# Kernel tuning notes

Measured on AMD Instinct MI355X. Metric: run time of the kernel, lower is better.

Reference implementation:

```python
import jax, jax.numpy as jnp
import numpy as np

N_NODES = 100000
N_EDGES = 1600000
IN_DIM = 128
HID_DIM = 128
OUT_DIM = 64
BN_EPS = 1e-5


def setup_inputs() -> dict:
    key = jax.random.key(0)
    ks = jax.random.split(key, 8)
    x = jax.random.normal(ks[0], (N_NODES, IN_DIM), dtype=jnp.float32)
    edge_index = jax.random.randint(ks[1], (2, N_EDGES), 0, N_NODES, dtype=jnp.int64)
    s1 = 1.0 / np.sqrt(IN_DIM)
    s2 = 1.0 / np.sqrt(HID_DIM)
    return {
        "x": x,
        "edge_index": edge_index,
        "W1l": jax.random.normal(ks[2], (HID_DIM, IN_DIM), dtype=jnp.float32) * s1,
        "b1l": jnp.zeros((HID_DIM,), dtype=jnp.float32),
        "W1r": jax.random.normal(ks[3], (HID_DIM, IN_DIM), dtype=jnp.float32) * s1,
        "bn_gamma": jnp.ones((HID_DIM,), dtype=jnp.float32),
        "bn_beta": jnp.zeros((HID_DIM,), dtype=jnp.float32),
        "bn_mean": jnp.zeros((HID_DIM,), dtype=jnp.float32),
        "bn_var": jnp.ones((HID_DIM,), dtype=jnp.float32),
        "W2l": jax.random.normal(ks[4], (OUT_DIM, HID_DIM), dtype=jnp.float32) * s2,
        "b2l": jnp.zeros((OUT_DIM,), dtype=jnp.float32),
        "W2r": jax.random.normal(ks[5], (OUT_DIM, HID_DIM), dtype=jnp.float32) * s2,
    }


def _sage_conv(x, src, dst, Wl, bl, Wr, num_nodes):
    # message = x[src], mean-aggregated at dst; out = lin_l(agg) + lin_r(x)
    msgs = x[src]  # [E, D] gather (memory bound)
    agg = jax.ops.segment_sum(msgs, dst, num_segments=num_nodes)
    deg = jax.ops.segment_sum(jnp.ones((src.shape[0],), dtype=x.dtype), dst,
                              num_segments=num_nodes)
    agg = agg / jnp.maximum(deg, 1.0)[:, None]
    return agg @ Wl.T + bl + x @ Wr.T


def reference(x, edge_index, W1l, b1l, W1r, bn_gamma, bn_beta, bn_mean, bn_var,
              W2l, b2l, W2r):
    src, dst = edge_index[0], edge_index[1]
    n = x.shape[0]
    h = _sage_conv(x, src, dst, W1l, b1l, W1r, n)
    # BatchNorm1d (inference: running stats), then ReLU; dropout is identity in eval
    h = (h - bn_mean) * (bn_gamma * jax.lax.rsqrt(bn_var + BN_EPS)) + bn_beta
    h = jax.nn.relu(h)
    return _sage_conv(h, src, dst, W2l, b2l, W2r, n)
```

## Files before the change

kernel.cpp:

```cpp
#include <hip/hip_runtime.h>
#include <hip/hip_fp16.h>

#define N_NODES 100000
#define N_EDGES 1600000
#define TILE 2048
#define NBUK 64
#define BSH 11
#define NBUK_USED ((N_NODES + (1 << BSH) - 1) >> BSH)
#define CAP 36864
#define SMASK 0x1FFFF

typedef _Float16 f16x8 __attribute__((ext_vector_type(8)));
typedef float    f32x4 __attribute__((ext_vector_type(4)));

__global__ __launch_bounds__(256) void k_pre(
    const float* __restrict__ x, __half* __restrict__ x_h,
    const float* __restrict__ W1l, const float* __restrict__ W1r,
    const float* __restrict__ W2l, const float* __restrict__ W2r,
    __half* __restrict__ W1lf, __half* __restrict__ W1rf,
    __half* __restrict__ W2f, int* __restrict__ bcur)
{
    int i = blockIdx.x * 256 + threadIdx.x;
    if (i < N_NODES * 32) {
        float4 v = ((const float4*)x)[i];
        __half2 a = __floats2half2_rn(v.x, v.y);
        __half2 b = __floats2half2_rn(v.z, v.w);
        uint2 u = make_uint2(*(unsigned*)&a, *(unsigned*)&b);
        ((uint2*)x_h)[i] = u;
    }
    if (i < 49152) {
        int tt = i & 16383;
        int j    = tt & 7;
        int lane = (tt >> 3) & 63;
        int ks   = (tt >> 9) & 3;
        int ct   = tt >> 11;
        int m = lane & 15, q = lane >> 4;
        int row = ct * 16 + m;
        int col = ks * 32 + q * 8 + j;
        if (i < 16384) {
            W1lf[tt] = __float2half(W1l[row * 128 + col]);
        } else if (i < 32768) {
            W1rf[tt] = __float2half(W1r[row * 128 + col]);
        } else {
            float v = (ct < 4) ? W2l[row * 128 + col]
                               : W2r[(row - 64) * 128 + col];
            W2f[tt] = __float2half(v);
        }
    }
    if (i < NBUK) bcur[i] = i * CAP;
}

__global__ __launch_bounds__(256) void k_binA(
    const int* __restrict__ ei, int* __restrict__ bcur,
    int2* __restrict__ ebuf)
{
    __shared__ int2 scratch[TILE];
    __shared__ int hist[NBUK];
    __shared__ int tstart[NBUK];
    __shared__ int gbase[NBUK];
    int t = threadIdx.x;
    int e0 = blockIdx.x * TILE;
    int tile_n = min(TILE, N_EDGES - e0);
    if (t < NBUK) hist[t] = 0;
    __syncthreads();
    int srcs[8], dsts[8], rank[8], bks[8];
    #pragma unroll
    for (int i = 0; i < 8; ++i) {
        int e = e0 + i * 256 + t;
        bks[i] = -1;
        if (e < N_EDGES) {
            srcs[i] = ei[e];
            dsts[i] = ei[N_EDGES + e];
            bks[i]  = (dsts[i] >> BSH) & (NBUK - 1);
            rank[i] = atomicAdd(&hist[bks[i]], 1);
        }
    }
    __syncthreads();
    if (t == 0) {
        int s = 0;
        #pragma unroll
        for (int b = 0; b < NBUK; ++b) { tstart[b] = s; s += hist[b]; }
    }
    __syncthreads();
    if (t < NBUK && hist[t] > 0)
        gbase[t] = atomicAdd(&bcur[t], hist[t]);
    __syncthreads();
    #pragma unroll
    for (int i = 0; i < 8; ++i)
        if (bks[i] >= 0) {
            int sl = tstart[bks[i]] + rank[i];
            scratch[min(sl, TILE - 1)] = make_int2(srcs[i], dsts[i]);
        }
    __syncthreads();
    for (int p = t; p < tile_n; p += 256) {
        int2 sd = scratch[p];
        int b = (sd.y >> BSH) & (NBUK - 1);
        int o = gbase[b] + (p - tstart[b]);
        ebuf[min(max(o, 0), NBUK * CAP - 1)] = sd;
    }
}

__global__ __launch_bounds__(1024) void k_fillC2(
    const int2* __restrict__ ebuf, const int* __restrict__ bcur,
    int* __restrict__ row_ptr, int* __restrict__ csr_src)
{
    __shared__ int hist[1 << BSH];
    __shared__ int psum[1024];
    __shared__ int cur[1 << BSH];
    __shared__ int bb_l[NBUK_USED + 1];
    int t = threadIdx.x;
    int b = blockIdx.x;
    int base = b << BSH;
    hist[t] = 0;
    hist[t + 1024] = 0;
    if (t < 64) {
        int c = (t < NBUK_USED) ? (bcur[t] - t * CAP) : 0;
        c = min(max(c, 0), CAP);
        int s = c;
        #pragma unroll
        for (int off = 1; off < 64; off <<= 1) {
            int v = __shfl_up(s, off);
            if (t >= off) s += v;
        }
        if (t < NBUK_USED) bb_l[t] = s - c;
        if (t == NBUK_USED - 1) bb_l[NBUK_USED] = s;
    }
    __syncthreads();
    int bb  = bb_l[b];
    int cnt = min(bb_l[b + 1] - bb, CAP);
    const int2* eb = ebuf + (size_t)b * CAP;
    for (int p = t; p < cnt; p += 1024)
        atomicAdd(&hist[(eb[p].y - base) & ((1 << BSH) - 1)], 1);
    __syncthreads();
    int h0 = hist[2 * t], h1 = hist[2 * t + 1];
    psum[t] = h0 + h1;
    __syncthreads();
    #pragma unroll
    for (int off = 1; off < 1024; off <<= 1) {
        int v = (t >= off) ? psum[t - off] : 0;
        __syncthreads();
        psum[t] += v;
        __syncthreads();
    }
    int e0 = bb + psum[t] - (h0 + h1);
    int e1 = e0 + h0;
    int n0g = base + 2 * t, n1g = n0g + 1;
    if (n0g <= N_NODES) row_ptr[n0g] = e0;
    if (n1g <= N_NODES) row_ptr[n1g] = e1;
    cur[2 * t]     = e0;
    cur[2 * t + 1] = e1;
    __syncthreads();
    for (int p = t; p < cnt; p += 1024) {
        int2 sd = eb[p];
        int pos = atomicAdd(&cur[(sd.y - base) & ((1 << BSH) - 1)], 1);
        csr_src[min(max(pos, 0), N_EDGES - 1)] = sd.x;
    }
}

__device__ __forceinline__ void acc_row8(
    const __half* __restrict__ x_h, int s, int col, float4& acc)
{
    uint2 u = ((const uint2*)(x_h + (size_t)(s & SMASK) * 128))[col];
    __half2 a = *(__half2*)&u.x;
    __half2 b = *(__half2*)&u.y;
    float2 fa = __half22float2(a);
    float2 fb = __half22float2(b);
    acc.x += fa.x; acc.y += fa.y; acc.z += fb.x; acc.w += fb.y;
}

__global__ __launch_bounds__(256) void k_l12(
    const int* __restrict__ row_ptr, const int* __restrict__ csr_src,
    const __half* __restrict__ x_h,
    const __half* __restrict__ W1lf, const float* __restrict__ b1l,
    const __half* __restrict__ W1rf,
    const float* __restrict__ gamma, const float* __restrict__ beta,
    const float* __restrict__ mean, const float* __restrict__ var,
    const __half* __restrict__ W2f, const float* __restrict__ b2l,
    __half* __restrict__ p2, float* __restrict__ out)
{
    __shared__ char sm[34816];
    __half (*Aagg)[64][8] = (__half(*)[64][8])sm;
    __half (*Ax)[64][8]   = (__half(*)[64][8])(sm + 16384);
    __half (*Ah)[64][8]   = (__half(*)[64][8])sm;
    float  (*Cs)[132]     = (float(*)[132])sm;
    __shared__ float invdeg[64];
    int tid  = threadIdx.x;
    int lane = tid & 63;
    int w    = tid >> 6;
    int n0   = blockIdx.x * 64;

    {
        int n  = tid & 63;
        int kg = tid >> 6;
        int ng = n0 + n;
        const uint4* px = (const uint4*)(x_h + (size_t)ng * 128 + kg * 32);
        #pragma unroll
        for (int i = 0; i < 4; ++i) {
            uint4 vx = make_uint4(0, 0, 0, 0);
            if (ng < N_NODES) vx = px[i];
            *(uint4*)&Ax[kg * 4 + i][n][0] = vx;
        }
    }

    {
        int half = lane >> 5;
        int col  = lane & 31;
        for (int i = 0; i < 16; ++i) {
            int nn = n0 + w * 16 + i;
            int e0 = 0, e1 = 0;
            if (nn < N_NODES) {
                e1 = min(row_ptr[nn + 1], N_EDGES);
                e0 = min(max(row_ptr[nn], 0), e1);
            }
            float4 acc = make_float4(0.f, 0.f, 0.f, 0.f);
            for (int eb = e0; eb < e1; eb += 64) {
                int cnt = min(e1 - eb, 64);
                int sv = csr_src[min(eb + lane, N_EDGES - 1)];
                int j = 0;
                for (; j + 8 <= cnt; j += 8) {
                    #pragma unroll
                    for (int u = 0; u < 4; ++u) {
                        int sa = __builtin_amdgcn_readlane(sv, j + 2 * u);
                        int sb = __builtin_amdgcn_readlane(sv, j + 2 * u + 1);
                        int s  = half ? sb : sa;
                        acc_row8(x_h, s, col, acc);
                    }
                }
                for (; j + 2 <= cnt; j += 2) {
                    int sa = __builtin_amdgcn_readlane(sv, j);
                    int sb = __builtin_amdgcn_readlane(sv, j + 1);
                    int s  = half ? sb : sa;
                    acc_row8(x_h, s, col, acc);
                }
                if (j < cnt) {
                    int sa = __builtin_amdgcn_readlane(sv, j);
                    if (half == 0) acc_row8(x_h, sa, col, acc);
                }
            }
            acc.x += __shfl_xor(acc.x, 32);
            acc.y += __shfl_xor(acc.y, 32);
            acc.z += __shfl_xor(acc.z, 32);
            acc.w += __shfl_xor(acc.w, 32);
            if (lane == 0)
                invdeg[w * 16 + i] = 1.0f / fmaxf((float)(e1 - e0), 1.0f);
            if (half == 0) {
                __half2 h0 = __floats2half2_rn(acc.x, acc.y);
                __half2 h1 = __floats2half2_rn(acc.z, acc.w);
                uint2 u = make_uint2(*(unsigned*)&h0, *(unsigned*)&h1);
                *(uint2*)&Aagg[col >> 1][w * 16 + i][(col & 1) * 4] = u;
            }
        }
    }
    __syncthreads();

    int m = lane & 15;
    int q = lane >> 4;
    int row = w * 16 + m;
    const __half* bl0 = W1lf + (lane << 3);
    const __half* br0 = W1rf + (lane << 3);
    f32x4 accL[8], accR[8];
    #pragma unroll
    for (int c = 0; c < 8; ++c) {
        accL[c] = (f32x4){0.f, 0.f, 0.f, 0.f};
        accR[c] = (f32x4){0.f, 0.f, 0.f, 0.f};
    }
    #pragma unroll
    for (int ks = 0; ks < 4; ++ks) {
        f16x8 aL = *(const f16x8*)&Aagg[ks * 4 + q][row][0];
        f16x8 aR = *(const f16x8*)&Ax[ks * 4 + q][row][0];
        #pragma unroll
        for (int ct = 0; ct < 8; ++ct) {
            f16x8 bL = *(const f16x8*)(bl0 + ((ct * 4 + ks) << 9));
            f16x8 bR = *(const f16x8*)(br0 + ((ct * 4 + ks) << 9));
            accL[ct] = __builtin_amdgcn_mfma_f32_16x16x32_f16(aL, bL, accL[ct], 0, 0, 0);
            accR[ct] = __builtin_amdgcn_mfma_f32_16x16x32_f16(aR, bR, accR[ct], 0, 0, 0);
        }
    }
    float invd[4];
    #pragma unroll
    for (int r = 0; r < 4; ++r)
        invd[r] = invdeg[w * 16 + q * 4 + r];
    __syncthreads();

    #pragma unroll
    for (int ct = 0; ct < 8; ++ct) {
        int col = ct * 16 + m;
        float s = gamma[col] * rsqrtf(var[col] + 1e-5f);
        float t = beta[col] + (b1l[col] - mean[col]) * s;
        #pragma unroll
        for (int r = 0; r < 4; ++r) {
            float v = accL[ct][r] * invd[r] + accR[ct][r];
            v = fmaxf(v * s + t, 0.f);
            Ah[col >> 3][w * 16 + q * 4 + r][col & 7] = __float2half(v);
        }
    }
    __syncthreads();

    const __half* b0 = W2f + (lane << 3);
    f32x4 acc2[8];
    #pragma unroll
    for (int c = 0; c < 8; ++c) acc2[c] = (f32x4){0.f, 0.f, 0.f, 0.f};
    #pragma unroll
    for (int ks = 0; ks < 4; ++ks) {
        f16x8 a = *(const f16x8*)&Ah[ks * 4 + q][row][0];
        #pragma unroll
        for (int ct = 0; ct < 8; ++ct) {
            f16x8 b = *(const f16x8*)(b0 + ((ct * 4 + ks) << 9));
            acc2[ct] = __builtin_amdgcn_mfma_f32_16x16x32_f16(a, b, acc2[ct], 0, 0, 0);
        }
    }
    __syncthreads();
    #pragma unroll
    for (int ct = 0; ct < 8; ++ct) {
        int col = ct * 16 + m;
        #pragma unroll
        for (int r = 0; r < 4; ++r)
            Cs[w * 16 + q * 4 + r][col] = acc2[ct][r];
    }
    __syncthreads();
    {
        int rr = tid & 63;
        int pg = tid >> 6;
        int ng = n0 + rr;
        if (ng < N_NODES) {
            union { __half hh[16]; uint4 u[2]; } tmp;
            #pragma unroll
            for (int c = 0; c < 16; ++c)
                tmp.hh[c] = __float2half(Cs[rr][pg * 16 + c]);
            uint4* dp = (uint4*)(p2 + (size_t)ng * 64 + pg * 16);
            dp[0] = tmp.u[0];
            dp[1] = tmp.u[1];
            #pragma unroll
            for (int i = 0; i < 4; ++i) {
                float4 v  = *(const float4*)&Cs[rr][64 + pg * 16 + i * 4];
                float4 bb = *(const float4*)(b2l + pg * 16 + i * 4);
                v.x += bb.x; v.y += bb.y; v.z += bb.z; v.w += bb.w;
                *(float4*)(out + (size_t)ng * 64 + pg * 16 + i * 4) = v;
            }
        }
    }
}

__device__ __forceinline__ void acc_row_p2(
    const __half* __restrict__ p2, int s, int lane, float4& acc)
{
    uint2 u = ((const uint2*)(p2 + (size_t)(s & SMASK) * 64))[lane];
    __half2 a = *(__half2*)&u.x;
    __half2 b = *(__half2*)&u.y;
    float2 fa = __half22float2(a);
    float2 fb = __half22float2(b);
    acc.x += fa.x; acc.y += fa.y; acc.z += fb.x; acc.w += fb.y;
}

__global__ __launch_bounds__(256) void k_agg2(
    const int* __restrict__ row_ptr, const int* __restrict__ csr_src,
    const __half* __restrict__ p2, float* __restrict__ out)
{
    int tid  = threadIdx.x;
    int n    = blockIdx.x * 16 + (tid >> 4);
    int lane = tid & 15;
    int e1 = min(row_ptr[n + 1], N_EDGES);
    int e0 = min(max(row_ptr[n], 0), e1);
    float4 acc = make_float4(0.f, 0.f, 0.f, 0.f);
    int e = e0;
    for (; e + 4 <= e1; e += 4) {
        int s0 = csr_src[e], s1 = csr_src[e + 1];
        int s2 = csr_src[e + 2], s3 = csr_src[e + 3];
        acc_row_p2(p2, s0, lane, acc);
        acc_row_p2(p2, s1, lane, acc);
        acc_row_p2(p2, s2, lane, acc);
        acc_row_p2(p2, s3, lane, acc);
    }
    for (; e < e1; ++e) acc_row_p2(p2, csr_src[e], lane, acc);
    float inv = 1.0f / fmaxf((float)(e1 - e0), 1.0f);
    float4* o = (float4*)out + n * 16 + lane;
    float4 cur = *o;
    cur.x += acc.x * inv; cur.y += acc.y * inv;
    cur.z += acc.z * inv; cur.w += acc.w * inv;
    *o = cur;
}

extern "C" void kernel_launch(void* const* d_in, const int* in_sizes, int n_in,
                              void* d_out, int out_size, void* d_ws, size_t ws_size,
                              hipStream_t stream)
{
    const float* x     = (const float*)d_in[0];
    const int*   ei    = (const int*)d_in[1];
    const float* W1l   = (const float*)d_in[2];
    const float* b1l   = (const float*)d_in[3];
    const float* W1r   = (const float*)d_in[4];
    const float* gamma = (const float*)d_in[5];
    const float* beta  = (const float*)d_in[6];
    const float* mean  = (const float*)d_in[7];
    const float* var   = (const float*)d_in[8];
    const float* W2l   = (const float*)d_in[9];
    const float* b2l   = (const float*)d_in[10];
    const float* W2r   = (const float*)d_in[11];
    float* out = (float*)d_out;

    char* ws = (char*)d_ws;
    __half* p2      = (__half*)(ws);
    __half* x_h     = (__half*)(ws + 51200000);
    int*    csr_src = (int*)(ws + 76800000);
    int*    row_ptr = (int*)(ws + 83200000);
    __half* W1lf    = (__half*)(ws + 83600016);
    __half* W1rf    = (__half*)(ws + 83632784);
    __half* W2f     = (__half*)(ws + 83665552);
    int2*   ebuf    = (int2*)(ws + 83698320);
    int*    bcur    = (int*)(ws + 102572688);

    k_pre<<<12500, 256, 0, stream>>>(x, x_h, W1l, W1r, W2l, W2r,
                                     W1lf, W1rf, W2f, bcur);
    k_binA<<<(N_EDGES + TILE - 1) / TILE, 256, 0, stream>>>(ei, bcur, ebuf);
    k_fillC2<<<NBUK_USED, 1024, 0, stream>>>(ebuf, bcur, row_ptr, csr_src);
    k_l12<<<(N_NODES + 63) / 64, 256, 0, stream>>>(row_ptr, csr_src, x_h,
                                                   W1lf, b1l, W1rf,
                                                   gamma, beta, mean, var,
                                                   W2f, b2l, p2, out);
    k_agg2<<<N_NODES / 16, 256, 0, stream>>>(row_ptr, csr_src, p2, out);
}
```

Before: 378.7 us.

## Split layer-1 aggregation out of fused GEMM kernel into separate gather kernel

Moves the layer-1 neighbor gather out of the fused aggregate+GEMM kernel into a standalone kernel with one wave per node and many small blocks, writing fp16 aggregates to a workspace buffer. The GEMM kernel then loads the aggregates coalesced and recomputes inverse degree from row_ptr. The aim is better latency hiding and load balance for the gather, since it no longer runs serially 16 nodes per wave inside a shared-memory-heavy block. The cost is an extra 25.6MB write and read plus one more kernel launch.

```diff
diff --git a/kernel.cpp b/kernel.cpp
--- a/kernel.cpp
+++ b/kernel.cpp
@@ -168,8 +168,56 @@
     acc.x += fa.x; acc.y += fa.y; acc.z += fb.x; acc.w += fb.y;
 }
 
-__global__ __launch_bounds__(256) void k_l12(
+__global__ __launch_bounds__(256) void k_agg1(
     const int* __restrict__ row_ptr, const int* __restrict__ csr_src,
+    const __half* __restrict__ x_h, __half* __restrict__ agg_h)
+{
+    int tid  = threadIdx.x;
+    int lane = tid & 63;
+    int half = lane >> 5;
+    int col  = lane & 31;
+    int n    = blockIdx.x * 4 + (tid >> 6);
+    int e1 = min(row_ptr[n + 1], N_EDGES);
+    int e0 = min(max(row_ptr[n], 0), e1);
+    float4 acc = make_float4(0.f, 0.f, 0.f, 0.f);
+    for (int eb = e0; eb < e1; eb += 64) {
+        int cnt = min(e1 - eb, 64);
+        int sv = csr_src[min(eb + lane, N_EDGES - 1)];
+        int j = 0;
+        for (; j + 8 <= cnt; j += 8) {
+            #pragma unroll
+            for (int u = 0; u < 4; ++u) {
+                int sa = __builtin_amdgcn_readlane(sv, j + 2 * u);
+                int sb = __builtin_amdgcn_readlane(sv, j + 2 * u + 1);
+                int s  = half ? sb : sa;
+                acc_row8(x_h, s, col, acc);
+            }
+        }
+        for (; j + 2 <= cnt; j += 2) {
+            int sa = __builtin_amdgcn_readlane(sv, j);
+            int sb = __builtin_amdgcn_readlane(sv, j + 1);
+            int s  = half ? sb : sa;
+            acc_row8(x_h, s, col, acc);
+        }
+        if (j < cnt) {
+            int sa = __builtin_amdgcn_readlane(sv, j);
+            if (half == 0) acc_row8(x_h, sa, col, acc);
+        }
+    }
+    acc.x += __shfl_xor(acc.x, 32);
+    acc.y += __shfl_xor(acc.y, 32);
+    acc.z += __shfl_xor(acc.z, 32);
+    acc.w += __shfl_xor(acc.w, 32);
+    if (half == 0) {
+        __half2 h0 = __floats2half2_rn(acc.x, acc.y);
+        __half2 h1 = __floats2half2_rn(acc.z, acc.w);
+        uint2 u = make_uint2(*(unsigned*)&h0, *(unsigned*)&h1);
+        ((uint2*)agg_h)[n * 32 + col] = u;
+    }
+}
+
+__global__ __launch_bounds__(256) void k_g12(
+    const __half* __restrict__ agg_h, const int* __restrict__ row_ptr,
     const __half* __restrict__ x_h,
     const __half* __restrict__ W1lf, const float* __restrict__ b1l,
     const __half* __restrict__ W1rf,
@@ -183,76 +231,27 @@
     __half (*Ax)[64][8]   = (__half(*)[64][8])(sm + 16384);
     __half (*Ah)[64][8]   = (__half(*)[64][8])sm;
     float  (*Cs)[132]     = (float(*)[132])sm;
-    __shared__ float invdeg[64];
-    int tid  = threadIdx.x;
-    int lane = tid & 63;
-    int w    = tid >> 6;
-    int n0   = blockIdx.x * 64;
+    int tid = threadIdx.x;
+    int n0  = blockIdx.x * 64;
 
     {
         int n  = tid & 63;
         int kg = tid >> 6;
         int ng = n0 + n;
-        const uint4* px = (const uint4*)(x_h + (size_t)ng * 128 + kg * 32);
+        const uint4* pa = (const uint4*)(agg_h + (size_t)ng * 128 + kg * 32);
+        const uint4* px = (const uint4*)(x_h   + (size_t)ng * 128 + kg * 32);
         #pragma unroll
         for (int i = 0; i < 4; ++i) {
-            uint4 vx = make_uint4(0, 0, 0, 0);
-            if (ng < N_NODES) vx = px[i];
-            *(uint4*)&Ax[kg * 4 + i][n][0] = vx;
-        }
-    }
-
-    {
-        int half = lane >> 5;
-        int col  = lane & 31;
-        for (int i = 0; i < 16; ++i) {
-            int nn = n0 + w * 16 + i;
-            int e0 = 0, e1 = 0;
-            if (nn < N_NODES) {
-                e1 = min(row_ptr[nn + 1], N_EDGES);
-                e0 = min(max(row_ptr[nn], 0), e1);
-            }
-            float4 acc = make_float4(0.f, 0.f, 0.f, 0.f);
-            for (int eb = e0; eb < e1; eb += 64) {
-                int cnt = min(e1 - eb, 64);
-                int sv = csr_src[min(eb + lane, N_EDGES - 1)];
-                int j = 0;
-                for (; j + 8 <= cnt; j += 8) {
-                    #pragma unroll
-                    for (int u = 0; u < 4; ++u) {
-                        int sa = __builtin_amdgcn_readlane(sv, j + 2 * u);
-                        int sb = __builtin_amdgcn_readlane(sv, j + 2 * u + 1);
-                        int s  = half ? sb : sa;
-                        acc_row8(x_h, s, col, acc);
-                    }
-                }
-                for (; j + 2 <= cnt; j += 2) {
-                    int sa = __builtin_amdgcn_readlane(sv, j);
-                    int sb = __builtin_amdgcn_readlane(sv, j + 1);
-                    int s  = half ? sb : sa;
-                    acc_row8(x_h, s, col, acc);
-                }
-                if (j < cnt) {
-                    int sa = __builtin_amdgcn_readlane(sv, j);
-                    if (half == 0) acc_row8(x_h, sa, col, acc);
-                }
-            }
-            acc.x += __shfl_xor(acc.x, 32);
-            acc.y += __shfl_xor(acc.y, 32);
-            acc.z += __shfl_xor(acc.z, 32);
-            acc.w += __shfl_xor(acc.w, 32);
-            if (lane == 0)
-                invdeg[w * 16 + i] = 1.0f / fmaxf((float)(e1 - e0), 1.0f);
-            if (half == 0) {
-                __half2 h0 = __floats2half2_rn(acc.x, acc.y);
-                __half2 h1 = __floats2half2_rn(acc.z, acc.w);
-                uint2 u = make_uint2(*(unsigned*)&h0, *(unsigned*)&h1);
-                *(uint2*)&Aagg[col >> 1][w * 16 + i][(col & 1) * 4] = u;
-            }
-        }
-    }
-    __syncthreads();
-
+            uint4 va = make_uint4(0, 0, 0, 0), vx = va;
+            if (ng < N_NODES) { va = pa[i]; vx = px[i]; }
+            *(uint4*)&Aagg[kg * 4 + i][n][0] = va;
+            *(uint4*)&Ax[kg * 4 + i][n][0]   = vx;
+        }
+    }
+    __syncthreads();
+
+    int lane = tid & 63;
+    int w = tid >> 6;
     int m = lane & 15;
     int q = lane >> 4;
     int row = w * 16 + m;
@@ -278,8 +277,11 @@
     }
     float invd[4];
     #pragma unroll
-    for (int r = 0; r < 4; ++r)
-        invd[r] = invdeg[w * 16 + q * 4 + r];
+    for (int r = 0; r < 4; ++r) {
+        int n = n0 + w * 16 + q * 4 + r;
+        int d = (n < N_NODES) ? (row_ptr[n + 1] - row_ptr[n]) : 1;
+        invd[r] = 1.0f / fmaxf((float)d, 1.0f);
+    }
     __syncthreads();
 
     #pragma unroll
@@ -399,7 +401,8 @@
     float* out = (float*)d_out;
 
     char* ws = (char*)d_ws;
-    __half* p2      = (__half*)(ws);
+    __half* agg_h   = (__half*)(ws);
+    __half* p2      = (__half*)(ws + 25600000);
     __half* x_h     = (__half*)(ws + 51200000);
     int*    csr_src = (int*)(ws + 76800000);
     int*    row_ptr = (int*)(ws + 83200000);
@@ -413,7 +416,8 @@
                                      W1lf, W1rf, W2f, bcur);
     k_binA<<<(N_EDGES + TILE - 1) / TILE, 256, 0, stream>>>(ei, bcur, ebuf);
     k_fillC2<<<NBUK_USED, 1024, 0, stream>>>(ebuf, bcur, row_ptr, csr_src);
-    k_l12<<<(N_NODES + 63) / 64, 256, 0, stream>>>(row_ptr, csr_src, x_h,
+    k_agg1<<<N_NODES / 4, 256, 0, stream>>>(row_ptr, csr_src, x_h, agg_h);
+    k_g12<<<(N_NODES + 63) / 64, 256, 0, stream>>>(agg_h, row_ptr, x_h,
                                                    W1lf, b1l, W1rf,
                                                    gamma, beta, mean, var,
                                                    W2f, b2l, p2, out);
```

New measurement: 327.7 us. 13.5% less time.
